# Performance work log

Measured on AMD Instinct MI355X. Metric: run time of the kernel, lower is better.

The kernel has to match this reference:

```python
import jax, jax.numpy as jnp
import numpy as np

B, C, HID, H, W = 4, 64, 64, 64, 64


def setup_inputs() -> dict:
    key = jax.random.key(0)
    ks = jax.random.split(key, 9)
    s_in = 1.0 / np.sqrt(C)
    return {
        "x": jax.random.normal(ks[0], (B, C, H, W), dtype=jnp.float32),
        "Wq": jax.random.normal(ks[1], (HID, C), dtype=jnp.float32) * s_in,
        "bq": jnp.zeros((HID,), dtype=jnp.float32),
        "Wk": jax.random.normal(ks[2], (HID, C), dtype=jnp.float32) * s_in,
        "bk": jnp.zeros((HID,), dtype=jnp.float32),
        "Wv": jax.random.normal(ks[3], (C, C), dtype=jnp.float32) * s_in,
        "bv": jnp.zeros((C,), dtype=jnp.float32),
        "Wo": jax.random.normal(ks[4], (1, C), dtype=jnp.float32) * s_in,
        "bo": jnp.zeros((1,), dtype=jnp.float32),
    }


def reference(x, Wq, bq, Wk, bk, Wv, bv, Wo, bo):
    b, c, h, w = x.shape
    n = h * w
    xf = x.reshape(b, c, n)                                   # [B,C,N]
    q = jnp.einsum('dc,bcn->bnd', Wq, xf) + bq                # [B,N,HID]
    k = jnp.einsum('dc,bcn->bdn', Wk, xf) + bk[None, :, None]  # [B,HID,N]
    v = jnp.einsum('ec,bcn->bne', Wv, xf) + bv                # [B,N,C]
    scale = 1.0 / jnp.sqrt(jnp.asarray(k.shape[1], x.dtype))
    attn = jax.nn.softmax(jnp.einsum('bnd,bdm->bnm', q, k) * scale, axis=-1)
    out = jnp.einsum('bnm,bme->bne', attn, v)                 # [B,N,C]
    out = out.transpose(0, 2, 1).reshape(b, c, h, w)
    y = jnp.einsum('oc,bchw->bohw', Wo, out) + bo[None, :, None, None]
    return jax.nn.sigmoid(y)
```

## Files before the change

kernel.cpp:

```cpp
#include <hip/hip_runtime.h>
#include <math.h>

#define NB 4
#define NN 4096
#define QSCALE 0.1803368801f

#define KS 16
#define KPB 256
#define STK 64
#define NST (KPB / STK)
#define NG 2
#define NQT (NB * 32)

typedef __bf16 bf16x8 __attribute__((ext_vector_type(8)));
typedef float f32x4 __attribute__((ext_vector_type(4)));
typedef float f32x2 __attribute__((ext_vector_type(2)));

union BF8 { unsigned short u[8]; bf16x8 v; uint4 q; };

static __device__ inline unsigned short f2bf(float f) {
    union { float f; unsigned u; } v; v.f = f;
    unsigned r = v.u + 0x7fffu + ((v.u >> 16) & 1u);
    return (unsigned short)(r >> 16);
}

__global__ __launch_bounds__(256) void prep_mfma(
    const float* __restrict__ x,
    const float* __restrict__ Wq, const float* __restrict__ bq,
    const float* __restrict__ Wk, const float* __restrict__ bk,
    const float* __restrict__ Wv, const float* __restrict__ bv,
    const float* __restrict__ Wo,
    unsigned short* __restrict__ Qb, unsigned short* __restrict__ Kb,
    float* __restrict__ VW)
{
    __shared__ float xt[64 * 33];
    __shared__ float wve_s[64];
    __shared__ unsigned short rows[4 * 16 * 72];

    const int blk = blockIdx.x;
    const int b = blk >> 7;
    const int n0 = (blk & 127) << 5;
    const int tid = threadIdx.x;
    const int wid = tid >> 6, lane = tid & 63;
    const int lg = lane >> 4, ll = lane & 15;

    const float* xb = x + (size_t)b * 64 * NN;
    #pragma unroll
    for (int it = 0; it < 8; ++it) {
        int idx = it * 256 + tid;
        int c = idx >> 5, n = idx & 31;
        xt[c * 33 + n] = xb[(size_t)c * NN + n0 + n];
    }
    {
        int c = tid >> 2, part = tid & 3;
        float a = 0.f;
        #pragma unroll
        for (int j = 0; j < 16; ++j) {
            int e = part * 16 + j;
            a = fmaf(Wo[e], Wv[e * 64 + c], a);
        }
        a += __shfl_xor(a, 1);
        a += __shfl_xor(a, 2);
        if (part == 0) wve_s[c] = a;
    }
    float cv;
    {
        float p = Wo[lane] * bv[lane];
        #pragma unroll
        for (int off = 1; off < 64; off <<= 1) p += __shfl_xor(p, off);
        cv = p;
    }
    __syncthreads();

    {
        int nrel = tid >> 3, part = tid & 7;
        float a = 0.f;
        #pragma unroll
        for (int j = 0; j < 8; ++j) {
            int c = part * 8 + j;
            a = fmaf(wve_s[c], xt[c * 33 + nrel], a);
        }
        a += __shfl_xor(a, 1);
        a += __shfl_xor(a, 2);
        a += __shfl_xor(a, 4);
        if (part == 0) VW[(size_t)b * NN + n0 + nrel] = a + cv;
    }

    const int nr = (wid & 1) * 16 + ll;
    BF8 a0, a1;
    #pragma unroll
    for (int j = 0; j < 8; ++j) {
        a0.v[j] = (__bf16)xt[(lg * 8 + j) * 33 + nr];
        a1.v[j] = (__bf16)xt[(32 + lg * 8 + j) * 33 + nr];
    }

    const float* W  = (wid < 2) ? Wq : Wk;
    const float* bs = (wid < 2) ? bq : bk;
    unsigned short* Out = (wid < 2) ? Qb : Kb;
    const float scale = (wid < 2) ? QSCALE : 1.f;
    unsigned short* myrows = rows + wid * (16 * 72);

    #pragma unroll
    for (int ct = 0; ct < 4; ++ct) {
        const float* wr = W + (ct * 16 + ll) * 64;
        float4 f0 = *(const float4*)(wr + lg * 8);
        float4 f1 = *(const float4*)(wr + lg * 8 + 4);
        float4 f2 = *(const float4*)(wr + 32 + lg * 8);
        float4 f3 = *(const float4*)(wr + 32 + lg * 8 + 4);
        BF8 w0, w1;
        w0.v[0] = (__bf16)f0.x; w0.v[1] = (__bf16)f0.y; w0.v[2] = (__bf16)f0.z; w0.v[3] = (__bf16)f0.w;
        w0.v[4] = (__bf16)f1.x; w0.v[5] = (__bf16)f1.y; w0.v[6] = (__bf16)f1.z; w0.v[7] = (__bf16)f1.w;
        w1.v[0] = (__bf16)f2.x; w1.v[1] = (__bf16)f2.y; w1.v[2] = (__bf16)f2.z; w1.v[3] = (__bf16)f2.w;
        w1.v[4] = (__bf16)f3.x; w1.v[5] = (__bf16)f3.y; w1.v[6] = (__bf16)f3.z; w1.v[7] = (__bf16)f3.w;
        f32x4 acc = {0.f, 0.f, 0.f, 0.f};
        acc = __builtin_amdgcn_mfma_f32_16x16x32_bf16(a0.v, w0.v, acc, 0, 0, 0);
        acc = __builtin_amdgcn_mfma_f32_16x16x32_bf16(a1.v, w1.v, acc, 0, 0, 0);
        float bias = bs[ct * 16 + ll];
        #pragma unroll
        for (int r = 0; r < 4; ++r)
            myrows[(lg * 4 + r) * 72 + ct * 16 + ll] = f2bf((acc[r] + bias) * scale);
    }
    {
        int n = lane >> 2, c16 = lane & 3;
        const uint4* sp = (const uint4*)&myrows[n * 72 + c16 * 16];
        uint4 v0 = sp[0], v1 = sp[1];
        uint4* dst = (uint4*)(Out + ((size_t)b * NN + n0 + (wid & 1) * 16 + n) * 64 + c16 * 16);
        dst[0] = v0; dst[1] = v1;
    }
}

__global__ __launch_bounds__(256) void attn_mfma(
    const unsigned short* __restrict__ Qb, const unsigned short* __restrict__ Kb,
    const float* __restrict__ VW, float2* __restrict__ P2)
{
    __shared__ unsigned short kbuf[2][STK * 64];
    __shared__ float vws[KPB];
    const int blk = blockIdx.x;
    const int ks = blk & (KS - 1);
    const int t = blk >> 4;
    const int b = t >> 5;
    const int q0 = (t & 31) << 7;
    const int tid = threadIdx.x;
    const int wid = tid >> 6, lane = tid & 63;
    const int lg = lane >> 4, ll = lane & 15;

    vws[tid] = VW[(size_t)b * NN + ks * KPB + tid];

    bf16x8 qfa[NG], qfb[NG];
    #pragma unroll
    for (int g = 0; g < NG; ++g) {
        const unsigned short* qp =
            Qb + ((size_t)b * NN + q0 + g * 64 + wid * 16 + ll) * 64 + lg * 8;
        qfa[g] = *(const bf16x8*)qp;
        qfb[g] = *(const bf16x8*)(qp + 32);
    }

    const char* kchunk = (const char*)(Kb + ((size_t)b * NN + ks * KPB) * 64);
    const int d0 = tid * 16, d1 = 4096 + tid * 16;
    const int sw0 = d0 ^ (((d0 >> 7) & 7) << 4);
    const int sw1 = d1 ^ (((d1 >> 7) & 7) << 4);
    const int c0 = (lg ^ (ll & 7)) & 7;
    const int c1 = ((lg + 4) ^ (ll & 7)) & 7;

    {
        uint4 r0 = *(const uint4*)(kchunk + d0);
        uint4 r1 = *(const uint4*)(kchunk + d1);
        *(uint4*)((char*)kbuf[0] + sw0) = r0;
        *(uint4*)((char*)kbuf[0] + sw1) = r1;
    }
    __syncthreads();

    f32x2 ZA[NG];
    #pragma unroll
    for (int g = 0; g < NG; ++g) ZA[g] = (f32x2){0.f, 0.f};

    int cur = 0;
    #pragma unroll 1
    for (int st = 0; st < NST; ++st) {
        uint4 r0, r1;
        const bool more = (st + 1 < NST);
        if (more) {
            const char* src = kchunk + (size_t)(st + 1) * 8192;
            r0 = *(const uint4*)(src + d0);
            r1 = *(const uint4*)(src + d1);
        }
        const char* kb = (const char*)kbuf[cur];
        #pragma unroll
        for (int kt = 0; kt < 4; ++kt) {
            const int rowb = (kt * 16 + ll) * 128;
            const bf16x8 k0 = *(const bf16x8*)(kb + rowb + (c0 << 4));
            const bf16x8 k1 = *(const bf16x8*)(kb + rowb + (c1 << 4));
            const float4 vv = *(const float4*)&vws[st * 64 + kt * 16 + lg * 4];
            const f32x2 w0 = {1.f, vv.x}, w1 = {1.f, vv.y};
            const f32x2 w2 = {1.f, vv.z}, w3 = {1.f, vv.w};
            #pragma unroll
            for (int g = 0; g < NG; ++g) {
                f32x4 acc = {0.f, 0.f, 0.f, 0.f};
                acc = __builtin_amdgcn_mfma_f32_16x16x32_bf16(k0, qfa[g], acc, 0, 0, 0);
                acc = __builtin_amdgcn_mfma_f32_16x16x32_bf16(k1, qfb[g], acc, 0, 0, 0);
                float e0 = __builtin_amdgcn_exp2f(acc[0]);
                float e1 = __builtin_amdgcn_exp2f(acc[1]);
                float e2 = __builtin_amdgcn_exp2f(acc[2]);
                float e3 = __builtin_amdgcn_exp2f(acc[3]);
                ZA[g] = __builtin_elementwise_fma((f32x2){e0, e0}, w0, ZA[g]);
                ZA[g] = __builtin_elementwise_fma((f32x2){e1, e1}, w1, ZA[g]);
                ZA[g] = __builtin_elementwise_fma((f32x2){e2, e2}, w2, ZA[g]);
                ZA[g] = __builtin_elementwise_fma((f32x2){e3, e3}, w3, ZA[g]);
            }
        }
        if (more) {
            char* dst = (char*)kbuf[cur ^ 1];
            *(uint4*)(dst + sw0) = r0;
            *(uint4*)(dst + sw1) = r1;
            __syncthreads();
            cur ^= 1;
        }
    }

    #pragma unroll
    for (int g = 0; g < NG; ++g) {
        float Z = ZA[g].x, A = ZA[g].y;
        Z += __shfl_xor(Z, 16); Z += __shfl_xor(Z, 32);
        A += __shfl_xor(A, 16); A += __shfl_xor(A, 32);
        if (lg == 0)
            P2[((size_t)ks << 14) + ((size_t)b << 12) + q0 + g * 64 + wid * 16 + ll] =
                make_float2(Z, A);
    }
}

__global__ __launch_bounds__(64) void combine_kernel(
    const float2* __restrict__ P2, const float* __restrict__ bo,
    float* __restrict__ out)
{
    int i = blockIdx.x * 64 + threadIdx.x;
    float Z = 0.f, A = 0.f;
    #pragma unroll
    for (int r = 0; r < KS; ++r) {
        float2 p = P2[((size_t)r << 14) + i];
        Z += p.x; A += p.y;
    }
    float y = A / Z + bo[0];
    out[i] = 1.f / (1.f + __expf(-y));
}

extern "C" void kernel_launch(void* const* d_in, const int* in_sizes, int n_in,
                              void* d_out, int out_size, void* d_ws, size_t ws_size,
                              hipStream_t stream)
{
    const float* x  = (const float*)d_in[0];
    const float* Wq = (const float*)d_in[1];
    const float* bq = (const float*)d_in[2];
    const float* Wk = (const float*)d_in[3];
    const float* bk = (const float*)d_in[4];
    const float* Wv = (const float*)d_in[5];
    const float* bv = (const float*)d_in[6];
    const float* Wo = (const float*)d_in[7];
    const float* bo = (const float*)d_in[8];
    float* out = (float*)d_out;

    unsigned short* Qb = (unsigned short*)d_ws;
    unsigned short* Kb = Qb + (size_t)NB * NN * 64;
    float* VW = (float*)(Kb + (size_t)NB * NN * 64);
    float2* P2 = (float2*)(VW + (size_t)NB * NN);

    prep_mfma<<<NB * 128, 256, 0, stream>>>(x, Wq, bq, Wk, bk, Wv, bv, Wo,
                                            Qb, Kb, VW);
    attn_mfma<<<NQT * KS, 256, 0, stream>>>(Qb, Kb, VW, P2);
    combine_kernel<<<(NB * NN) / 64, 64, 0, stream>>>(P2, bo, out);
}
```

Baseline: 33.53 us.

## Halve prep tile to 16 positions, split output channels across waves

The projection prep kernel now handles 16 spatial positions per block instead of 32, so it launches twice as many blocks. Each wave computes half the output channels of Q or K instead of all of them for a half-tile. x is loaded with float4 vector reads and the LDS padding is reduced. The goal is more parallelism and better memory-level concurrency in the small prep kernel, at the cost of reading the weights redundantly across more blocks.

```diff
diff --git a/kernel.cpp b/kernel.cpp
--- a/kernel.cpp
+++ b/kernel.cpp
@@ -33,23 +33,21 @@
     unsigned short* __restrict__ Qb, unsigned short* __restrict__ Kb,
     float* __restrict__ VW)
 {
-    __shared__ float xt[64 * 33];
+    __shared__ float xt[64 * 20];
     __shared__ float wve_s[64];
-    __shared__ unsigned short rows[4 * 16 * 72];
+    __shared__ unsigned short rows[4][16 * 40];
 
     const int blk = blockIdx.x;
-    const int b = blk >> 7;
-    const int n0 = (blk & 127) << 5;
+    const int b = blk >> 8;
+    const int n0 = (blk & 255) << 4;
     const int tid = threadIdx.x;
     const int wid = tid >> 6, lane = tid & 63;
     const int lg = lane >> 4, ll = lane & 15;
 
-    const float* xb = x + (size_t)b * 64 * NN;
-    #pragma unroll
-    for (int it = 0; it < 8; ++it) {
-        int idx = it * 256 + tid;
-        int c = idx >> 5, n = idx & 31;
-        xt[c * 33 + n] = xb[(size_t)c * NN + n0 + n];
+    {
+        int c = tid >> 2, nq = tid & 3;
+        float4 v = *(const float4*)(x + (size_t)b * 64 * NN + (size_t)c * NN + n0 + nq * 4);
+        *(float4*)&xt[c * 20 + nq * 4] = v;
     }
     {
         int c = tid >> 2, part = tid & 3;
@@ -73,35 +71,38 @@
     __syncthreads();
 
     {
-        int nrel = tid >> 3, part = tid & 7;
+        int pos = tid >> 4, part = tid & 15;
         float a = 0.f;
         #pragma unroll
-        for (int j = 0; j < 8; ++j) {
-            int c = part * 8 + j;
-            a = fmaf(wve_s[c], xt[c * 33 + nrel], a);
+        for (int j = 0; j < 4; ++j) {
+            int c = part * 4 + j;
+            a = fmaf(wve_s[c], xt[c * 20 + pos], a);
         }
         a += __shfl_xor(a, 1);
         a += __shfl_xor(a, 2);
         a += __shfl_xor(a, 4);
-        if (part == 0) VW[(size_t)b * NN + n0 + nrel] = a + cv;
-    }
-
-    const int nr = (wid & 1) * 16 + ll;
+        a += __shfl_xor(a, 8);
+        if (part == 0) VW[(size_t)b * NN + n0 + pos] = a + cv;
+    }
+
     BF8 a0, a1;
     #pragma unroll
     for (int j = 0; j < 8; ++j) {
-        a0.v[j] = (__bf16)xt[(lg * 8 + j) * 33 + nr];
-        a1.v[j] = (__bf16)xt[(32 + lg * 8 + j) * 33 + nr];
-    }
-
-    const float* W  = (wid < 2) ? Wq : Wk;
-    const float* bs = (wid < 2) ? bq : bk;
-    unsigned short* Out = (wid < 2) ? Qb : Kb;
-    const float scale = (wid < 2) ? QSCALE : 1.f;
-    unsigned short* myrows = rows + wid * (16 * 72);
-
-    #pragma unroll
-    for (int ct = 0; ct < 4; ++ct) {
+        a0.v[j] = (__bf16)xt[(lg * 8 + j) * 20 + ll];
+        a1.v[j] = (__bf16)xt[(32 + lg * 8 + j) * 20 + ll];
+    }
+
+    const int proj = wid >> 1;
+    const int ctbase = (wid & 1) * 2;
+    const float* W  = proj ? Wk : Wq;
+    const float* bs = proj ? bk : bq;
+    unsigned short* Out = proj ? Kb : Qb;
+    const float scale = proj ? 1.f : QSCALE;
+    unsigned short* myrows = rows[wid];
+
+    #pragma unroll
+    for (int cc = 0; cc < 2; ++cc) {
+        int ct = ctbase + cc;
         const float* wr = W + (ct * 16 + ll) * 64;
         float4 f0 = *(const float4*)(wr + lg * 8);
         float4 f1 = *(const float4*)(wr + lg * 8 + 4);
@@ -118,14 +119,12 @@
         float bias = bs[ct * 16 + ll];
         #pragma unroll
         for (int r = 0; r < 4; ++r)
-            myrows[(lg * 4 + r) * 72 + ct * 16 + ll] = f2bf((acc[r] + bias) * scale);
-    }
-    {
-        int n = lane >> 2, c16 = lane & 3;
-        const uint4* sp = (const uint4*)&myrows[n * 72 + c16 * 16];
-        uint4 v0 = sp[0], v1 = sp[1];
-        uint4* dst = (uint4*)(Out + ((size_t)b * NN + n0 + (wid & 1) * 16 + n) * 64 + c16 * 16);
-        dst[0] = v0; dst[1] = v1;
+            myrows[(lg * 4 + r) * 40 + cc * 16 + ll] = f2bf((acc[r] + bias) * scale);
+    }
+    {
+        int pos = lane >> 2, seg = lane & 3;
+        uint4 v = *(const uint4*)&myrows[pos * 40 + seg * 8];
+        *(uint4*)(Out + ((size_t)b * NN + n0 + pos) * 64 + ctbase * 16 + seg * 8) = v;
     }
 }
 
@@ -263,7 +262,7 @@
     float* VW = (float*)(Kb + (size_t)NB * NN * 64);
     float2* P2 = (float2*)(VW + (size_t)NB * NN);
 
-    prep_mfma<<<NB * 128, 256, 0, stream>>>(x, Wq, bq, Wk, bk, Wv, bv, Wo,
+    prep_mfma<<<NB * 256, 256, 0, stream>>>(x, Wq, bq, Wk, bk, Wv, bv, Wo,
                                             Qb, Kb, VW);
     attn_mfma<<<NQT * KS, 256, 0, stream>>>(Qb, Kb, VW, P2);
     combine_kernel<<<(NB * NN) / 64, 64, 0, stream>>>(P2, bo, out);
```

After: 34.97 us. 1.04x slower.

## Fuse split-K combine into attention kernel via last-block atomic ticket

Applied to the files above, without the earlier changes.

Drops the separate combine kernel launch. Each attention block now writes its partial (Z, A) with atomic stores and increments a per-query-tile counter, and the last of the KS split blocks reduces the partials and writes the sigmoid output. The counters are reset inside the prep kernel. This saves a launch and the gap between kernels, at the cost of an atomic and an extra barrier per block, plus a serialized tail reduction in the last block of each tile.

```diff
diff --git a/kernel.cpp b/kernel.cpp
--- a/kernel.cpp
+++ b/kernel.cpp
@@ -17,6 +17,7 @@
 typedef float f32x2 __attribute__((ext_vector_type(2)));
 
 union BF8 { unsigned short u[8]; bf16x8 v; uint4 q; };
+union F2U { float2 f; unsigned long long u; };
 
 static __device__ inline unsigned short f2bf(float f) {
     union { float f; unsigned u; } v; v.f = f;
@@ -31,7 +32,7 @@
     const float* __restrict__ Wv, const float* __restrict__ bv,
     const float* __restrict__ Wo,
     unsigned short* __restrict__ Qb, unsigned short* __restrict__ Kb,
-    float* __restrict__ VW)
+    float* __restrict__ VW, int* __restrict__ tick)
 {
     __shared__ float xt[64 * 33];
     __shared__ float wve_s[64];
@@ -43,6 +44,8 @@
     const int tid = threadIdx.x;
     const int wid = tid >> 6, lane = tid & 63;
     const int lg = lane >> 4, ll = lane & 15;
+
+    if (blk == 0 && tid < NQT) tick[tid * 32] = 0;
 
     const float* xb = x + (size_t)b * 64 * NN;
     #pragma unroll
@@ -131,10 +134,12 @@
 
 __global__ __launch_bounds__(256) void attn_mfma(
     const unsigned short* __restrict__ Qb, const unsigned short* __restrict__ Kb,
-    const float* __restrict__ VW, float2* __restrict__ P2)
+    const float* __restrict__ VW, const float* __restrict__ bo,
+    float2* __restrict__ P2, int* __restrict__ tick, float* __restrict__ out)
 {
     __shared__ unsigned short kbuf[2][STK * 64];
     __shared__ float vws[KPB];
+    __shared__ int lastflag;
     const int blk = blockIdx.x;
     const int ks = blk & (KS - 1);
     const int t = blk >> 4;
@@ -222,25 +227,34 @@
         float Z = ZA[g].x, A = ZA[g].y;
         Z += __shfl_xor(Z, 16); Z += __shfl_xor(Z, 32);
         A += __shfl_xor(A, 16); A += __shfl_xor(A, 32);
-        if (lg == 0)
-            P2[((size_t)ks << 14) + ((size_t)b << 12) + q0 + g * 64 + wid * 16 + ll] =
-                make_float2(Z, A);
-    }
-}
-
-__global__ __launch_bounds__(64) void combine_kernel(
-    const float2* __restrict__ P2, const float* __restrict__ bo,
-    float* __restrict__ out)
-{
-    int i = blockIdx.x * 64 + threadIdx.x;
-    float Z = 0.f, A = 0.f;
-    #pragma unroll
-    for (int r = 0; r < KS; ++r) {
-        float2 p = P2[((size_t)r << 14) + i];
-        Z += p.x; A += p.y;
-    }
-    float y = A / Z + bo[0];
-    out[i] = 1.f / (1.f + __expf(-y));
+        if (lg == 0) {
+            F2U u; u.f = make_float2(Z, A);
+            __hip_atomic_store(
+                (unsigned long long*)&P2[((size_t)t * KS + ks) * 128 + g * 64 + wid * 16 + ll],
+                u.u, __ATOMIC_RELAXED, __HIP_MEMORY_SCOPE_AGENT);
+        }
+    }
+    __syncthreads();
+    if (tid == 0) {
+        int old = __hip_atomic_fetch_add(&tick[t * 32], 1, __ATOMIC_ACQ_REL,
+                                         __HIP_MEMORY_SCOPE_AGENT);
+        lastflag = (old == KS - 1);
+    }
+    __syncthreads();
+
+    if (lastflag && tid < 128) {
+        float Z = 0.f, A = 0.f;
+        #pragma unroll
+        for (int r = 0; r < KS; ++r) {
+            F2U u;
+            u.u = __hip_atomic_load(
+                (unsigned long long*)&P2[((size_t)t * KS + r) * 128 + tid],
+                __ATOMIC_RELAXED, __HIP_MEMORY_SCOPE_AGENT);
+            Z += u.f.x; A += u.f.y;
+        }
+        float y = A / Z + bo[0];
+        out[(size_t)b * NN + q0 + tid] = 1.f / (1.f + __expf(-y));
+    }
 }
 
 extern "C" void kernel_launch(void* const* d_in, const int* in_sizes, int n_in,
@@ -262,9 +276,9 @@
     unsigned short* Kb = Qb + (size_t)NB * NN * 64;
     float* VW = (float*)(Kb + (size_t)NB * NN * 64);
     float2* P2 = (float2*)(VW + (size_t)NB * NN);
+    int* tick = (int*)(P2 + (size_t)NQT * KS * 128);
 
     prep_mfma<<<NB * 128, 256, 0, stream>>>(x, Wq, bq, Wk, bk, Wv, bv, Wo,
-                                            Qb, Kb, VW);
-    attn_mfma<<<NQT * KS, 256, 0, stream>>>(Qb, Kb, VW, P2);
-    combine_kernel<<<(NB * NN) / 64, 64, 0, stream>>>(P2, bo, out);
-}
+                                            Qb, Kb, VW, tick);
+    attn_mfma<<<NQT * KS, 256, 0, stream>>>(Qb, Kb, VW, bo, P2, tick, out);
+}
```

Result: slower. 66.58 us (+98.6%).
